# Optimization experiments

Measured on AMD Instinct MI355X. Metric: run time of the kernel, lower is better.

Reference implementation:

```python
import jax, jax.numpy as jnp
import numpy as np

HID, HEADS = 2048, 16
Q_LORA, KV_LORA = 1536, 512
NOPE, ROPE, VD = 128, 64, 128
N_EXP, TOPK, MOE_I, SH_I = 8, 2, 1408, 2816
EPS, RSF = 1e-6, 1.0
ROPE_BASE = 10000.0


def _rms(x, w):
    return x * jax.lax.rsqrt(jnp.mean(jnp.square(x), -1, keepdims=True) + EPS) * w


def _rope(x, pos):
    # neox-style rotary on last dim; x: [T, H, d], pos: [T]
    d = x.shape[-1]
    inv = 1.0 / (ROPE_BASE ** (jnp.arange(0, d, 2, dtype=jnp.float32) / d))
    ang = pos.astype(jnp.float32)[:, None] * inv  # [T, d/2]
    cos, sin = jnp.cos(ang)[:, None, :], jnp.sin(ang)[:, None, :]
    x1, x2 = x[..., : d // 2], x[..., d // 2:]
    return jnp.concatenate([x1 * cos - x2 * sin, x2 * cos + x1 * sin], -1)


def setup_inputs() -> dict:
    key = jax.random.key(0)
    ks = jax.random.split(key, 16)
    T, s, f = 1024, 0.02, jnp.float32
    return {
        'positions': jnp.arange(T, dtype=jnp.int32),
        'hidden_states': jax.random.normal(ks[0], (T, HID), f),
        'residual': jax.random.normal(ks[1], (T, HID), f),
        'w_in_ln': jnp.ones((HID,), f),
        'w_post_ln': jnp.ones((HID,), f),
        'w_q_ln': jnp.ones((Q_LORA,), f),
        'w_kv_ln': jnp.ones((KV_LORA,), f),
        'w_qkv_a': jax.random.normal(ks[2], (HID, Q_LORA + KV_LORA + ROPE), f) * s,
        'w_q_b': jax.random.normal(ks[3], (Q_LORA, HEADS * (NOPE + ROPE)), f) * s,
        'w_kv_b': jax.random.normal(ks[4], (KV_LORA, HEADS * (NOPE + VD)), f) * s,
        'w_o': jax.random.normal(ks[5], (HEADS * VD, HID), f) * s,
        'gate_w': jax.random.normal(ks[6], (HID, N_EXP), f) * s,
        'we_gate': jax.random.normal(ks[7], (N_EXP, HID, MOE_I), f) * s,
        'we_up': jax.random.normal(ks[8], (N_EXP, HID, MOE_I), f) * s,
        'we_down': jax.random.normal(ks[9], (N_EXP, MOE_I, HID), f) * s,
        'ws_gate': jax.random.normal(ks[10], (HID, SH_I), f) * s,
        'ws_up': jax.random.normal(ks[11], (HID, SH_I), f) * s,
        'ws_down': jax.random.normal(ks[12], (SH_I, HID), f) * s,
    }


def reference(positions, hidden_states, residual, w_in_ln, w_post_ln, w_q_ln, w_kv_ln,
              w_qkv_a, w_q_b, w_kv_b, w_o, gate_w, we_gate, we_up, we_down,
              ws_gate, ws_up, ws_down):
    T = hidden_states.shape[0]
    # fused_add_rms_norm: residual <- x + residual; x <- rmsnorm(residual)
    residual = hidden_states + residual
    h = _rms(residual, w_in_ln)
    # fused qkv_a projection and split
    qkv = h @ w_qkv_a  # [T, q_lora + kv_lora + rope]
    q_c = _rms(qkv[:, :Q_LORA], w_q_ln)
    kv_c = _rms(qkv[:, Q_LORA:Q_LORA + KV_LORA], w_kv_ln)
    k_pe = qkv[:, Q_LORA + KV_LORA:][:, None, :]  # [T, 1, rope]
    # MLA up-projections
    q = (q_c @ w_q_b).reshape(T, HEADS, NOPE + ROPE)
    q_nope, q_pe = q[..., :NOPE], q[..., NOPE:]
    kv = (kv_c @ w_kv_b).reshape(T, HEADS, NOPE + VD)
    k_nope, v = kv[..., :NOPE], kv[..., NOPE:]
    q_pe = _rope(q_pe, positions)
    k_pe = _rope(k_pe, positions)
    q = jnp.concatenate([q_nope, q_pe], -1)  # [T, H, nope+rope]
    k = jnp.concatenate([k_nope, jnp.broadcast_to(k_pe, (T, HEADS, ROPE))], -1)
    scores = jnp.einsum('qhd,khd->hqk', q, k) * (NOPE + ROPE) ** -0.5
    causal = jnp.tril(jnp.ones((T, T), bool))
    scores = jnp.where(causal, scores, jnp.finfo(scores.dtype).min)
    p = jax.nn.softmax(scores, -1)
    attn_out = jnp.einsum('hqk,khd->qhd', p, v).reshape(T, HEADS * VD) @ w_o
    # post-attention fused add + norm
    residual = residual + attn_out
    h = _rms(residual, w_post_ln)
    # MoE gate: softmax scores, top-k, renormalized combine weights
    probs = jax.nn.softmax(h @ gate_w, -1)
    tw, ti = jax.lax.top_k(probs, TOPK)
    tw = tw / jnp.sum(tw, -1, keepdims=True)
    comb = jnp.sum(jax.nn.one_hot(ti, N_EXP, dtype=h.dtype) * tw[..., None], 1)  # [T, E]
    # routed experts (dense grouped-GEMM reference, SwiGLU)
    g = jnp.einsum('th,ehi->eti', h, we_gate)
    u = jnp.einsum('th,ehi->eti', h, we_up)
    y = jnp.einsum('eti,eih->eth', jax.nn.silu(g) * u, we_down)
    routed = jnp.einsum('te,eth->th', comb, y) * RSF
    # shared experts
    shared = (jax.nn.silu(h @ ws_gate) * (h @ ws_up)) @ ws_down
    return routed + shared, residual
```

## Files before the change

kernel.cpp:

```cpp
#include <hip/hip_runtime.h>
#include <hip/hip_bf16.h>

typedef unsigned short u16;
typedef __attribute__((ext_vector_type(8))) short bf16x8;
typedef __attribute__((ext_vector_type(4))) float f32x4;
typedef __attribute__((ext_vector_type(8))) unsigned short u16x8;
typedef __attribute__((ext_vector_type(4))) unsigned short u16x4;

#define T_TOK 1024
#define HID 2048
#define HEADS 16
#define Q_LORA 1536
#define KV_LORA 512
#define NOPE 128
#define ROPED 64
#define VD 128
#define N_EXP 8
#define MOE_I 1408
#define SH_I 2816
#define QKV_N 2112
#define QKV_LD 2176
#define QD 192
#define KVD 256
#define EPSF 1e-6f
#define NEG_BIG (-3.4e38f)

__device__ __forceinline__ u16 f2bf(float f) {
  union { float f; unsigned u; } x; x.f = f;
  unsigned r = x.u + 0x7fffu + ((x.u >> 16) & 1u);
  return (u16)(r >> 16);
}
__device__ __forceinline__ float bf2f(u16 h) {
  union { unsigned u; float f; } x; x.u = ((unsigned)h) << 16; return x.f;
}
__device__ __forceinline__ void split2(float f, u16& hi, u16& lo) {
  hi = f2bf(f);
  lo = f2bf(f - bf2f(hi));
}

__device__ __forceinline__ void gload16(const u16* g, const u16* l) {
  __builtin_amdgcn_global_load_lds(
      (const __attribute__((address_space(1))) void*)g,
      (__attribute__((address_space(3))) void*)l, 16, 0, 0);
}

__device__ __forceinline__ float block_sum(float v, float* s) {
  #pragma unroll
  for (int o = 32; o > 0; o >>= 1) v += __shfl_down(v, o, 64);
  int w = threadIdx.x >> 6, lane = threadIdx.x & 63;
  __syncthreads();
  if (lane == 0) s[w] = v;
  __syncthreads();
  float r = s[0];
  for (int i = 1; i < 4; ++i) r += s[i];
  return r;
}
__device__ __forceinline__ float block_max(float v, float* s) {
  #pragma unroll
  for (int o = 32; o > 0; o >>= 1) v = fmaxf(v, __shfl_down(v, o, 64));
  int w = threadIdx.x >> 6, lane = threadIdx.x & 63;
  __syncthreads();
  if (lane == 0) s[w] = v;
  __syncthreads();
  float r = s[0];
  for (int i = 1; i < 4; ++i) r = fmaxf(r, s[i]);
  return r;
}

__global__ __launch_bounds__(256) void gemm_bf16(
    const u16* __restrict__ A, long asz, int lda,
    const u16* __restrict__ B, long bsz, int ldb,
    float* __restrict__ C, u16* __restrict__ Cb, long csz, int ldc,
    const float* __restrict__ Cadd, const u16* __restrict__ CaddB, int ldcadd,
    int K, float alpha, int causal, int mode,
    float* __restrict__ pbuf, int ksplit, int stot, int soff,
    const int* __restrict__ gidx, const int* __restrict__ gcnt) {
  const int bm = blockIdx.y << 7, bn = blockIdx.x << 7;
  const int zz = blockIdx.z;
  const int z = (ksplit > 1) ? (zz / ksplit) : zz;
  const int s = (ksplit > 1) ? (zz % ksplit) : 0;
  if (gcnt && bm >= gcnt[z]) return;
  A += (long)z * asz; B += (long)z * bsz;
  if (C) C += (long)z * csz;
  if (Cb) Cb += (long)z * csz;
  if (Cadd && !pbuf) Cadd += (long)z * csz;
  if (CaddB) CaddB += (long)z * csz;
  const int tid = threadIdx.x, lane = tid & 63, wid = tid >> 6;

  if (causal && bn >= bm + 128) return;

  __shared__ alignas(16) u16 As[2][128 * 32];
  __shared__ alignas(16) u16 Bs[2][128 * 32];

  const int wr = wid >> 1, wc = wid & 1;
  f32x4 acc[4][4];
  #pragma unroll
  for (int m = 0; m < 4; ++m)
    #pragma unroll
    for (int n = 0; n < 4; ++n) acc[m][n] = f32x4{0.f, 0.f, 0.f, 0.f};

  const int srow = (wid << 5) + (lane >> 2);
  const int scol = (lane & 3) << 3;
  const int arow = (wr << 6) + (lane & 15);
  const int brow = (wc << 6) + (lane & 15);
  const int koff = (lane >> 4) << 3;

  long ga0, ga1;
  {
    if (gidx) {
      const int* tk = gidx + (long)z * T_TOK;
      ga0 = (long)tk[bm + srow]; ga1 = (long)tk[bm + srow + 16];
    } else {
      ga0 = (long)(bm + srow); ga1 = (long)(bm + srow + 16);
    }
  }

  const int kseg = K / ksplit;
  const int kbeg = s * kseg;
  const int nIter = kseg >> 5;

  #define STAGE_TILE(BUF, KK)                                                 \
    {                                                                         \
      u16* asp = &As[(BUF)][(wid << 10)];                                     \
      u16* bsp = &Bs[(BUF)][(wid << 10)];                                     \
      gload16(A + ga0 * lda + (KK) + scol, asp);                              \
      gload16(A + ga1 * lda + (KK) + scol, asp + 512);                        \
      gload16(B + (long)(bn + srow) * ldb + (KK) + scol, bsp);                \
      gload16(B + (long)(bn + srow + 16) * ldb + (KK) + scol, bsp + 512);     \
    }

  STAGE_TILE(0, kbeg);
  __syncthreads();

  int cur = 0;
  for (int it = 0; it < nIter; ++it) {
    int k0 = kbeg + (it << 5);
    if (it + 1 < nIter) STAGE_TILE(cur ^ 1, k0 + 32);
    bf16x8 a[4], b[4];
    #pragma unroll
    for (int m = 0; m < 4; ++m) a[m] = *(const bf16x8*)&As[cur][((arow + (m << 4)) << 5) + koff];
    #pragma unroll
    for (int n = 0; n < 4; ++n) b[n] = *(const bf16x8*)&Bs[cur][((brow + (n << 4)) << 5) + koff];
    #pragma unroll
    for (int m = 0; m < 4; ++m)
      #pragma unroll
      for (int n = 0; n < 4; ++n)
        acc[m][n] = __builtin_amdgcn_mfma_f32_16x16x32_bf16(a[m], b[n], acc[m][n], 0, 0, 0);
    __syncthreads();
    cur ^= 1;
  }
  #undef STAGE_TILE

  const int rbase = bm + (wr << 6) + ((lane >> 4) << 2);
  const int cbase = bn + (wc << 6) + (lane & 15);

  if (pbuf) {
    long pstride = (long)(gridDim.y << 7) * ldc;
    float* pp = pbuf + ((long)z * stot + soff + s) * pstride;
    #pragma unroll
    for (int m = 0; m < 4; ++m)
      #pragma unroll
      for (int j = 0; j < 4; ++j) {
        int r = rbase + (m << 4) + j;
        #pragma unroll
        for (int n = 0; n < 4; ++n) {
          int cc = cbase + (n << 4);
          pp[(long)r * ldc + cc] = acc[m][n][j];
        }
      }
    return;
  }

  #pragma unroll
  for (int m = 0; m < 4; ++m) {
    #pragma unroll
    for (int j = 0; j < 4; ++j) {
      int r = rbase + (m << 4) + j;
      #pragma unroll
      for (int n = 0; n < 4; ++n) {
        int cc = cbase + (n << 4);
        float v = acc[m][n][j] * alpha;
        if (mode == 0) {
          if (Cadd) v += Cadd[(long)r * ldcadd + cc];
          if (causal && cc > r) v = NEG_BIG;
          C[(long)r * ldc + cc] = v;
        } else if (mode == 1) {
          float gg = Cadd[(long)r * ldcadd + cc];
          float sgv = gg / (1.f + expf(-gg));
          Cb[(long)r * ldc + cc] = f2bf(sgv * v);
        } else if (mode == 2) {
          Cb[(long)r * ldc + cc] = f2bf(v);
        } else {
          float gg = bf2f(CaddB[(long)r * ldcadd + cc]);
          float sgv = gg / (1.f + expf(-gg));
          Cb[(long)r * ldc + cc] = f2bf(sgv * v);
        }
      }
    }
  }
}

__global__ __launch_bounds__(256) void reduce_sk(
    const float* __restrict__ pbuf, long pstride, int S,
    float* __restrict__ C, u16* __restrict__ Cb, long csz, int ldc, int Nc,
    const float* __restrict__ Cadd, long caddsz, int ldcadd,
    float alpha, int mode) {
  const int z = blockIdx.y;
  const float* pz = pbuf + (long)z * S * pstride;
  long idx = ((long)blockIdx.x * 256 + threadIdx.x) * 8;
  long r = idx / Nc; int c = (int)(idx - r * Nc);
  float a[8] = {0.f, 0.f, 0.f, 0.f, 0.f, 0.f, 0.f, 0.f};
  for (int s = 0; s < S; ++s) {
    const float* pp = pz + (long)s * pstride + idx;
    float4 x = *(const float4*)pp;
    float4 y = *(const float4*)(pp + 4);
    a[0] += x.x; a[1] += x.y; a[2] += x.z; a[3] += x.w;
    a[4] += y.x; a[5] += y.y; a[6] += y.z; a[7] += y.w;
  }
  long ob = (long)z * csz + r * ldc + c;
  if (mode == 0) {
    #pragma unroll
    for (int k = 0; k < 8; ++k) {
      float v = a[k] * alpha;
      if (Cadd) v += Cadd[(long)z * caddsz + r * ldcadd + c + k];
      C[ob + k] = v;
    }
  } else {
    u16x8 o;
    #pragma unroll
    for (int k = 0; k < 8; ++k) {
      float gg = Cadd[(long)z * caddsz + r * ldcadd + c + k];
      float sgv = gg / (1.f + expf(-gg));
      o[k] = f2bf(sgv * a[k] * alpha);
    }
    *(u16x8*)&Cb[ob] = o;
  }
}

__global__ __launch_bounds__(256) void transpose_f32_bf16(
    const float* __restrict__ src, long sbs, int ld_src, int Cvalid,
    u16* __restrict__ dst, long dbs, int ld_dst) {
  __shared__ float tile[64][65];
  src += (long)blockIdx.z * sbs; dst += (long)blockIdx.z * dbs;
  const int c0 = blockIdx.x << 6, r0 = blockIdx.y << 6;
  const int tid = threadIdx.x;
  const int tc = (tid & 15) << 2, tr0 = tid >> 4;
  const bool valid = c0 < Cvalid;
  #pragma unroll
  for (int i = 0; i < 4; ++i) {
    int r = tr0 + (i << 4);
    float4 v;
    if (valid) v = *(const float4*)&src[(long)(r0 + r) * ld_src + c0 + tc];
    else { v.x = 0.f; v.y = 0.f; v.z = 0.f; v.w = 0.f; }
    tile[r][tc] = v.x; tile[r][tc + 1] = v.y; tile[r][tc + 2] = v.z; tile[r][tc + 3] = v.w;
  }
  __syncthreads();
  const int oc = tid >> 2, seg = tid & 3;
  u16x8 o0, o1;
  #pragma unroll
  for (int k = 0; k < 8; ++k) o0[k] = f2bf(tile[(seg << 4) + k][oc]);
  #pragma unroll
  for (int k = 0; k < 8; ++k) o1[k] = f2bf(tile[(seg << 4) + 8 + k][oc]);
  u16* dp = &dst[(long)(c0 + oc) * ld_dst + r0 + (seg << 4)];
  *(u16x8*)dp = o0;
  *(u16x8*)(dp + 8) = o1;
}

__global__ __launch_bounds__(256) void transpose_split3(
    const float* __restrict__ src, long sbs, int ld_src, int Cvalid,
    u16* __restrict__ dst, long dbs, int Kp) {
  __shared__ float tile[64][65];
  src += (long)blockIdx.z * sbs; dst += (long)blockIdx.z * dbs;
  const int c0 = blockIdx.x << 6, r0 = blockIdx.y << 6;
  const int tid = threadIdx.x;
  const int tc = (tid & 15) << 2, tr0 = tid >> 4;
  const bool valid = c0 < Cvalid;
  #pragma unroll
  for (int i = 0; i < 4; ++i) {
    int r = tr0 + (i << 4);
    float4 v;
    if (valid) v = *(const float4*)&src[(long)(r0 + r) * ld_src + c0 + tc];
    else { v.x = 0.f; v.y = 0.f; v.z = 0.f; v.w = 0.f; }
    tile[r][tc] = v.x; tile[r][tc + 1] = v.y; tile[r][tc + 2] = v.z; tile[r][tc + 3] = v.w;
  }
  __syncthreads();
  const int oc = tid >> 2, seg = tid & 3;
  u16x8 h0, h1, l0, l1;
  #pragma unroll
  for (int k = 0; k < 8; ++k) {
    u16 hi, lo; split2(tile[(seg << 4) + k][oc], hi, lo);
    h0[k] = hi; l0[k] = lo;
  }
  #pragma unroll
  for (int k = 0; k < 8; ++k) {
    u16 hi, lo; split2(tile[(seg << 4) + 8 + k][oc], hi, lo);
    h1[k] = hi; l1[k] = lo;
  }
  const int ldd = 3 * Kp;
  u16* dp = &dst[(long)(c0 + oc) * ldd + r0 + (seg << 4)];
  *(u16x8*)dp = h0;            *(u16x8*)(dp + 8) = h1;
  *(u16x8*)(dp + Kp) = h0;     *(u16x8*)(dp + Kp + 8) = h1;
  *(u16x8*)(dp + 2 * Kp) = l0; *(u16x8*)(dp + 2 * Kp + 8) = l1;
}

__global__ __launch_bounds__(256) void conv_split3_kernel(
    const float* __restrict__ src, u16* __restrict__ dst, int C, long n) {
  long stride = (long)gridDim.x * 2048;
  for (long i = ((long)blockIdx.x * 256 + threadIdx.x) * 8; i < n; i += stride) {
    long r = i / C; int c = (int)(i - r * C);
    float4 a = *(const float4*)&src[i];
    float4 b = *(const float4*)&src[i + 4];
    u16x8 hv, lv;
    u16 hi, lo;
    split2(a.x, hi, lo); hv[0] = hi; lv[0] = lo;
    split2(a.y, hi, lo); hv[1] = hi; lv[1] = lo;
    split2(a.z, hi, lo); hv[2] = hi; lv[2] = lo;
    split2(a.w, hi, lo); hv[3] = hi; lv[3] = lo;
    split2(b.x, hi, lo); hv[4] = hi; lv[4] = lo;
    split2(b.y, hi, lo); hv[5] = hi; lv[5] = lo;
    split2(b.z, hi, lo); hv[6] = hi; lv[6] = lo;
    split2(b.w, hi, lo); hv[7] = hi; lv[7] = lo;
    u16* base = dst + r * (long)(3 * C) + c;
    *(u16x8*)base = hv;
    *(u16x8*)(base + C) = lv;
    *(u16x8*)(base + 2 * C) = hv;
  }
}

__global__ __launch_bounds__(256) void add_rms_kernel(
    const float* __restrict__ hs, const float* __restrict__ res,
    const float* __restrict__ w, float* __restrict__ resid1, u16* __restrict__ h3) {
  __shared__ float sbuf[4];
  int t = blockIdx.x;
  float v[8]; float ss = 0.f;
  #pragma unroll
  for (int i = 0; i < 8; ++i) {
    int j = threadIdx.x + (i << 8);
    float x = hs[(long)t * HID + j] + res[(long)t * HID + j];
    v[i] = x; resid1[(long)t * HID + j] = x; ss += x * x;
  }
  ss = block_sum(ss, sbuf);
  float sc = rsqrtf(ss / (float)HID + EPSF);
  u16* base = h3 + (long)t * (3 * HID);
  #pragma unroll
  for (int i = 0; i < 8; ++i) {
    int j = threadIdx.x + (i << 8);
    u16 hi, lo; split2(v[i] * sc * w[j], hi, lo);
    base[j] = hi; base[HID + j] = lo; base[2 * HID + j] = hi;
  }
}

template <int NW, bool SPLIT, bool WF32>
__global__ __launch_bounds__(256) void rms_rows_kernel(
    const float* __restrict__ in, int ldin, const float* __restrict__ w,
    u16* __restrict__ outb, float* __restrict__ outf) {
  __shared__ float sbuf[4];
  int t = blockIdx.x;
  const int W = NW * 256;
  float v[NW]; float ss = 0.f;
  #pragma unroll
  for (int i = 0; i < NW; ++i) {
    int j = threadIdx.x + (i << 8);
    float x = in[(long)t * ldin + j];
    v[i] = x; ss += x * x;
  }
  ss = block_sum(ss, sbuf);
  float sc = rsqrtf(ss / (float)W + EPSF);
  #pragma unroll
  for (int i = 0; i < NW; ++i) {
    int j = threadIdx.x + (i << 8);
    float y = v[i] * sc * w[j];
    if (SPLIT) {
      u16 hi, lo; split2(y, hi, lo);
      u16* base = outb + (long)t * (3 * W);
      base[j] = hi; base[W + j] = lo; base[2 * W + j] = hi;
    } else {
      outb[(long)t * W + j] = f2bf(y);
    }
    if (WF32) outf[(long)t * W + j] = y;
  }
}

__global__ __launch_bounds__(256) void rope_kernel(
    const int* __restrict__ pos, float* __restrict__ q,
    const float* __restrict__ qkv, float* __restrict__ kpe) {
  int t = blockIdx.x;
  float fp = (float)pos[t];
  for (int item = threadIdx.x; item < 544; item += 256) {
    int i = item & 31;
    float inv = expf(-((float)i * (2.f / 64.f)) * 9.210340371976184f);
    float ang = fp * inv;
    float c = cosf(ang), s = sinf(ang);
    if (item < 512) {
      int hh = item >> 5;
      long base = (long)t * (HEADS * QD) + hh * QD + NOPE;
      float x1 = q[base + i], x2 = q[base + 32 + i];
      q[base + i] = x1 * c - x2 * s;
      q[base + 32 + i] = x2 * c + x1 * s;
    } else {
      long base = (long)t * QKV_LD + (Q_LORA + KV_LORA);
      float x1 = qkv[base + i], x2 = qkv[base + 32 + i];
      kpe[(long)t * 64 + i] = x1 * c - x2 * s;
      kpe[(long)t * 64 + 32 + i] = x2 * c + x1 * s;
    }
  }
}

__global__ __launch_bounds__(192) void build_q3_kernel(
    const float* __restrict__ qbuf, u16* __restrict__ q3) {
  int t = blockIdx.x, h = blockIdx.y, d = threadIdx.x;
  float x = qbuf[(long)t * (HEADS * QD) + h * QD + d];
  u16 hi, lo; split2(x, hi, lo);
  u16* base = q3 + ((long)h * T_TOK + t) * (3 * QD);
  base[d] = hi; base[QD + d] = lo; base[2 * QD + d] = hi;
}

__global__ __launch_bounds__(192) void build_kmat3_kernel(
    const float* __restrict__ kv, const float* __restrict__ kpe,
    u16* __restrict__ kmat3) {
  int t = blockIdx.x, h = blockIdx.y, d = threadIdx.x;
  float v = (d < NOPE) ? kv[(long)t * (HEADS * KVD) + h * KVD + d]
                       : kpe[(long)t * 64 + (d - NOPE)];
  u16 hi, lo; split2(v, hi, lo);
  u16* base = kmat3 + ((long)h * T_TOK + t) * (3 * QD);
  base[d] = hi; base[QD + d] = hi; base[2 * QD + d] = lo;
}

__global__ __launch_bounds__(256) void softmax_kernel(
    const float* __restrict__ S, u16* __restrict__ P2) {
  __shared__ float sbuf[4];
  long row = blockIdx.x;
  int r = (int)(row & (T_TOK - 1));
  const float* p = S + row * T_TOK;
  float4 v = ((const float4*)p)[threadIdx.x];
  int c0 = threadIdx.x << 2;
  if (c0 + 0 > r) v.x = NEG_BIG;
  if (c0 + 1 > r) v.y = NEG_BIG;
  if (c0 + 2 > r) v.z = NEG_BIG;
  if (c0 + 3 > r) v.w = NEG_BIG;
  float m = fmaxf(fmaxf(v.x, v.y), fmaxf(v.z, v.w));
  m = block_max(m, sbuf);
  v.x = expf(v.x - m); v.y = expf(v.y - m); v.z = expf(v.z - m); v.w = expf(v.w - m);
  float s = v.x + v.y + v.z + v.w;
  s = block_sum(s, sbuf);
  float inv = 1.f / s;
  u16x4 hv, lv;
  u16 hi, lo;
  split2(v.x * inv, hi, lo); hv[0] = hi; lv[0] = lo;
  split2(v.y * inv, hi, lo); hv[1] = hi; lv[1] = lo;
  split2(v.z * inv, hi, lo); hv[2] = hi; lv[2] = lo;
  split2(v.w * inv, hi, lo); hv[3] = hi; lv[3] = lo;
  u16* base = P2 + row * (2 * T_TOK) + (threadIdx.x << 2);
  *(u16x4*)base = hv;
  *(u16x4*)(base + T_TOK) = lv;
}

__global__ __launch_bounds__(256) void gate_topk_kernel(
    const float* __restrict__ h2, const float* __restrict__ gw,
    int* __restrict__ ti, float* __restrict__ tw) {
  __shared__ float sbuf[4];
  __shared__ float lg[N_EXP];
  int t = blockIdx.x;
  float p[N_EXP] = {0.f, 0.f, 0.f, 0.f, 0.f, 0.f, 0.f, 0.f};
  for (int j = threadIdx.x; j < HID; j += 256) {
    float x = h2[(long)t * HID + j];
    const float* gr = gw + (long)j * N_EXP;
    #pragma unroll
    for (int e = 0; e < N_EXP; ++e) p[e] += x * gr[e];
  }
  #pragma unroll
  for (int e = 0; e < N_EXP; ++e) {
    float s = block_sum(p[e], sbuf);
    if (threadIdx.x == 0) lg[e] = s;
  }
  __syncthreads();
  if (threadIdx.x == 0) {
    float m = lg[0];
    for (int e = 1; e < N_EXP; ++e) m = fmaxf(m, lg[e]);
    float pe[N_EXP]; float s = 0.f;
    for (int e = 0; e < N_EXP; ++e) { pe[e] = expf(lg[e] - m); s += pe[e]; }
    for (int e = 0; e < N_EXP; ++e) pe[e] /= s;
    int i0 = 0;
    for (int e = 1; e < N_EXP; ++e) if (pe[e] > pe[i0]) i0 = e;
    int i1 = -1;
    for (int e = 0; e < N_EXP; ++e) if (e != i0 && (i1 < 0 || pe[e] > pe[i1])) i1 = e;
    float ssum = pe[i0] + pe[i1];
    ti[2 * t] = i0; ti[2 * t + 1] = i1;
    tw[2 * t] = pe[i0] / ssum; tw[2 * t + 1] = pe[i1] / ssum;
  }
}

__global__ __launch_bounds__(64) void route_build_kernel(
    const int* __restrict__ ti, int* __restrict__ tokidx,
    int* __restrict__ pos, int* __restrict__ cnt) {
  int e = blockIdx.x;
  int le = (e < 10) ? e : e - 10;
  int lane = threadIdx.x;
  if (le >= N_EXP) {
    for (int p = lane; p < T_TOK; p += 64) tokidx[(long)e * T_TOK + p] = p;
    if (lane == 0) cnt[e] = T_TOK;
    return;
  }
  int c = 0;
  for (int base = 0; base < T_TOK; base += 64) {
    int t = base + lane;
    int e0 = ti[2 * t], e1 = ti[2 * t + 1];
    bool match = (e0 == le) || (e1 == le);
    unsigned long long mask = __ballot(match);
    int pref = __popcll(mask & ((1ull << lane) - 1ull));
    if (match) {
      int p = c + pref;
      tokidx[(long)e * T_TOK + p] = t;
      if (e < 10) pos[2 * t + ((e0 == le) ? 0 : 1)] = p;
    }
    c += __popcll(mask);
  }
  for (int p = c + lane; p < T_TOK; p += 64) tokidx[(long)e * T_TOK + p] = 0;
  if (lane == 0) cnt[e] = c;
}

__global__ __launch_bounds__(256) void silu_mul_moe_kernel(
    const u16* __restrict__ gug, const int* __restrict__ cnt,
    u16* __restrict__ gact) {
  int r = blockIdx.x, e = blockIdx.y;
  int padded = (cnt[e] + 127) & ~127;
  if (r >= padded) return;
  int j = threadIdx.x << 3;
  if (j >= MOE_I) return;
  u16x8 gv = *(const u16x8*)&gug[((long)e * T_TOK + r) * MOE_I + j];
  u16x8 uv = *(const u16x8*)&gug[(((long)e + 10) * T_TOK + r) * MOE_I + j];
  u16x8 o;
  #pragma unroll
  for (int k = 0; k < 8; ++k) {
    float g = bf2f(gv[k]);
    o[k] = f2bf(g / (1.f + expf(-g)) * bf2f(uv[k]));
  }
  *(u16x8*)&gact[((long)e * T_TOK + r) * MOE_I + j] = o;
}

__global__ __launch_bounds__(256) void combine_out_kernel(
    const u16* __restrict__ y, const int* __restrict__ ti,
    const float* __restrict__ tw, const int* __restrict__ pos,
    float* __restrict__ out0) {
  int t = blockIdx.x;
  int j = threadIdx.x << 3;
  int e0 = ti[2 * t], e1 = ti[2 * t + 1];
  int p0 = pos[2 * t], p1 = pos[2 * t + 1];
  float w0 = tw[2 * t], w1 = tw[2 * t + 1];
  u16x8 a = *(const u16x8*)&y[((long)e0 * T_TOK + p0) * HID + j];
  u16x8 b = *(const u16x8*)&y[((long)e1 * T_TOK + p1) * HID + j];
  u16x8 c = *(const u16x8*)&y[((long)8 * T_TOK + t) * HID + j];
  u16x8 d = *(const u16x8*)&y[((long)9 * T_TOK + t) * HID + j];
  float* rp = out0 + (long)t * HID + j;
  #pragma unroll
  for (int k = 0; k < 8; ++k)
    rp[k] = w0 * bf2f(a[k]) + w1 * bf2f(b[k]) + bf2f(c[k]) + bf2f(d[k]);
}

extern "C" void kernel_launch(void* const* d_in, const int* in_sizes, int n_in,
                              void* d_out, int out_size, void* d_ws, size_t ws_size,
                              hipStream_t stream) {
  (void)in_sizes; (void)n_in; (void)out_size; (void)ws_size;
  const int*   positions = (const int*)d_in[0];
  const float* hs        = (const float*)d_in[1];
  const float* res       = (const float*)d_in[2];
  const float* w_in_ln   = (const float*)d_in[3];
  const float* w_post_ln = (const float*)d_in[4];
  const float* w_q_ln    = (const float*)d_in[5];
  const float* w_kv_ln   = (const float*)d_in[6];
  const float* w_qkv_a   = (const float*)d_in[7];
  const float* w_q_b     = (const float*)d_in[8];
  const float* w_kv_b    = (const float*)d_in[9];
  const float* w_o       = (const float*)d_in[10];
  const float* gate_w    = (const float*)d_in[11];
  const float* we_gate   = (const float*)d_in[12];
  const float* we_up     = (const float*)d_in[13];
  const float* we_down   = (const float*)d_in[14];
  const float* ws_gate   = (const float*)d_in[15];
  const float* ws_up     = (const float*)d_in[16];
  const float* ws_dn     = (const float*)d_in[17];

  float* out0   = (float*)d_out;
  float* resid2 = out0 + (long)T_TOK * HID;

  char* Wb = (char*)d_ws;
  size_t off = 0;
  #define CARVE(name, type, bytes) type* name = (type*)(Wb + off); off += (((size_t)(bytes) + 255) & ~(size_t)255)

  CARVE(wqkvaT3, u16, (size_t)QKV_LD * 3 * HID * 2);
  CARVE(wqbT3,   u16, (size_t)(HEADS * QD) * 3 * Q_LORA * 2);
  CARVE(wkvbT3,  u16, (size_t)(HEADS * KVD) * 3 * KV_LORA * 2);
  CARVE(woT3,    u16, (size_t)HID * 3 * HID * 2);

  size_t pool = off;
  CARVE(resid1, float, (size_t)T_TOK * HID * 4);
  CARVE(h3,     u16,   (size_t)T_TOK * 3 * HID * 2);
  CARVE(qkv,    float, (size_t)T_TOK * QKV_LD * 4);
  CARVE(qc3,    u16,   (size_t)T_TOK * 3 * Q_LORA * 2);
  CARVE(kvc3,   u16,   (size_t)T_TOK * 3 * KV_LORA * 2);
  CARVE(qbuf,   float, (size_t)T_TOK * HEADS * QD * 4);
  CARVE(q3,     u16,   (size_t)HEADS * T_TOK * 3 * QD * 2);
  CARVE(kvbuf,  float, (size_t)T_TOK * HEADS * KVD * 4);
  CARVE(kpe,    float, (size_t)T_TOK * 64 * 4);
  CARVE(kmat3,  u16,   (size_t)HEADS * T_TOK * 3 * QD * 2);
  CARVE(vt3,    u16,   (size_t)HEADS * VD * 3 * T_TOK * 2);
  CARVE(scores, float, (size_t)HEADS * T_TOK * T_TOK * 4);
  CARVE(P2,     u16,   (size_t)HEADS * T_TOK * 2 * T_TOK * 2);
  CARVE(attn,   float, (size_t)T_TOK * HID * 4);
  CARVE(attn3,  u16,   (size_t)T_TOK * 3 * HID * 2);
  size_t endA = off;
  float* pbufA = scores;

  off = pool;
  CARVE(wegu20, u16, (size_t)20 * MOE_I * HID * 2);
  CARVE(wedT10, u16, (size_t)10 * HID * MOE_I * 2);
  CARVE(h2,     float, (size_t)T_TOK * HID * 4);
  CARVE(h2_b,   u16,   (size_t)T_TOK * HID * 2);
  CARVE(ti,     int,   (size_t)T_TOK * 2 * 4);
  CARVE(tw,     float, (size_t)T_TOK * 2 * 4);
  CARVE(pos,    int,   (size_t)T_TOK * 2 * 4);
  CARVE(tokidx20, int, (size_t)20 * T_TOK * 4);
  CARVE(cnt20,  int,   128);
  CARVE(gug20,  u16,   (size_t)20 * T_TOK * MOE_I * 2);
  CARVE(gact,   u16,   (size_t)10 * T_TOK * MOE_I * 2);
  CARVE(ycomp,  u16,   (size_t)10 * T_TOK * HID * 2);
  if (off < endA) off = endA;
  #undef CARVE

  u16* wegT10 = wegu20;
  u16* weuT10 = wegu20 + (size_t)10 * MOE_I * HID;

  const float* nullf = nullptr;
  float* nullC = nullptr;
  u16* nullB = nullptr;
  const u16* nullBB = nullptr;
  const int* nullI = nullptr;

  hipLaunchKernelGGL(transpose_split3, dim3(QKV_LD / 64, HID / 64, 1), dim3(256), 0, stream,
                     w_qkv_a, 0L, QKV_N, QKV_N, wqkvaT3, 0L, HID);
  hipLaunchKernelGGL(transpose_split3, dim3(HEADS * QD / 64, Q_LORA / 64, 1), dim3(256), 0, stream,
                     w_q_b, 0L, HEADS * QD, HEADS * QD, wqbT3, 0L, Q_LORA);
  hipLaunchKernelGGL(transpose_split3, dim3(HEADS * KVD / 64, KV_LORA / 64, 1), dim3(256), 0, stream,
                     w_kv_b, 0L, HEADS * KVD, HEADS * KVD, wkvbT3, 0L, KV_LORA);
  hipLaunchKernelGGL(transpose_split3, dim3(HID / 64, HID / 64, 1), dim3(256), 0, stream,
                     w_o, 0L, HID, HID, woT3, 0L, HID);

  hipLaunchKernelGGL(add_rms_kernel, dim3(T_TOK), dim3(256), 0, stream,
                     hs, res, w_in_ln, resid1, h3);
  hipLaunchKernelGGL(gemm_bf16, dim3(QKV_LD / 128, T_TOK / 128, 4), dim3(256), 0, stream,
                     h3, 0L, 3 * HID, wqkvaT3, 0L, 3 * HID,
                     nullC, nullB, 0L, QKV_LD, nullf, nullBB, 0, 3 * HID, 1.f, 0, 0,
                     pbufA, 4, 4, 0, nullI, nullI);
  hipLaunchKernelGGL(reduce_sk, dim3(T_TOK * QKV_LD / 2048, 1), dim3(256), 0, stream,
                     pbufA, (long)T_TOK * QKV_LD, 4,
                     qkv, nullB, 0L, QKV_LD, QKV_LD, nullf, 0L, 0, 1.f, 0);
  hipLaunchKernelGGL((rms_rows_kernel<6, true, false>), dim3(T_TOK), dim3(256), 0, stream,
                     qkv, QKV_LD, w_q_ln, qc3, (float*)nullptr);
  hipLaunchKernelGGL((rms_rows_kernel<2, true, false>), dim3(T_TOK), dim3(256), 0, stream,
                     qkv + Q_LORA, QKV_LD, w_kv_ln, kvc3, (float*)nullptr);
  hipLaunchKernelGGL(gemm_bf16, dim3(HEADS * QD / 128, T_TOK / 128, 4), dim3(256), 0, stream,
                     qc3, 0L, 3 * Q_LORA, wqbT3, 0L, 3 * Q_LORA,
                     nullC, nullB, 0L, HEADS * QD, nullf, nullBB, 0, 3 * Q_LORA, 1.f, 0, 0,
                     pbufA, 4, 4, 0, nullI, nullI);
  hipLaunchKernelGGL(reduce_sk, dim3(T_TOK * HEADS * QD / 2048, 1), dim3(256), 0, stream,
                     pbufA, (long)T_TOK * HEADS * QD, 4,
                     qbuf, nullB, 0L, HEADS * QD, HEADS * QD, nullf, 0L, 0, 1.f, 0);
  hipLaunchKernelGGL(gemm_bf16, dim3(HEADS * KVD / 128, T_TOK / 128, 4), dim3(256), 0, stream,
                     kvc3, 0L, 3 * KV_LORA, wkvbT3, 0L, 3 * KV_LORA,
                     nullC, nullB, 0L, HEADS * KVD, nullf, nullBB, 0, 3 * KV_LORA, 1.f, 0, 0,
                     pbufA, 4, 4, 0, nullI, nullI);
  hipLaunchKernelGGL(reduce_sk, dim3(T_TOK * HEADS * KVD / 2048, 1), dim3(256), 0, stream,
                     pbufA, (long)T_TOK * HEADS * KVD, 4,
                     kvbuf, nullB, 0L, HEADS * KVD, HEADS * KVD, nullf, 0L, 0, 1.f, 0);
  hipLaunchKernelGGL(rope_kernel, dim3(T_TOK), dim3(256), 0, stream,
                     positions, qbuf, qkv, kpe);
  hipLaunchKernelGGL(build_q3_kernel, dim3(T_TOK, HEADS), dim3(192), 0, stream, qbuf, q3);
  hipLaunchKernelGGL(build_kmat3_kernel, dim3(T_TOK, HEADS), dim3(192), 0, stream,
                     kvbuf, kpe, kmat3);
  hipLaunchKernelGGL(transpose_split3, dim3(VD / 64, T_TOK / 64, HEADS), dim3(256), 0, stream,
                     kvbuf + NOPE, 256L, HEADS * KVD, VD, vt3, (long)VD * 3 * T_TOK, T_TOK);
  hipLaunchKernelGGL(gemm_bf16, dim3(T_TOK / 128, T_TOK / 128, HEADS), dim3(256), 0, stream,
                     q3, (long)T_TOK * 3 * QD, 3 * QD,
                     kmat3, (long)T_TOK * 3 * QD, 3 * QD,
                     scores, nullB, (long)T_TOK * T_TOK, T_TOK,
                     nullf, nullBB, 0, 576, 0.07216878364870322f, 1, 0,
                     nullC, 1, 1, 0, nullI, nullI);
  hipLaunchKernelGGL(softmax_kernel, dim3(HEADS * T_TOK), dim3(256), 0, stream, scores, P2);
  hipLaunchKernelGGL(gemm_bf16, dim3(VD / 128, T_TOK / 128, HEADS * 4), dim3(256), 0, stream,
                     P2, (long)T_TOK * 2 * T_TOK, 2 * T_TOK,
                     vt3, (long)VD * 3 * T_TOK, 3 * T_TOK,
                     nullC, nullB, 0L, VD, nullf, nullBB, 0, 2 * T_TOK, 1.f, 0, 0,
                     pbufA, 4, 6, 0, nullI, nullI);
  hipLaunchKernelGGL(gemm_bf16, dim3(VD / 128, T_TOK / 128, HEADS * 2), dim3(256), 0, stream,
                     P2, (long)T_TOK * 2 * T_TOK, 2 * T_TOK,
                     vt3 + 2 * T_TOK, (long)VD * 3 * T_TOK, 3 * T_TOK,
                     nullC, nullB, 0L, VD, nullf, nullBB, 0, T_TOK, 1.f, 0, 0,
                     pbufA, 2, 6, 4, nullI, nullI);
  hipLaunchKernelGGL(reduce_sk, dim3(T_TOK * VD / 2048, HEADS), dim3(256), 0, stream,
                     pbufA, (long)T_TOK * VD, 6,
                     attn, nullB, (long)VD, HID, VD, nullf, 0L, 0, 1.f, 0);
  hipLaunchKernelGGL(conv_split3_kernel, dim3(1024), dim3(256), 0, stream,
                     attn, attn3, HID, (long)T_TOK * HID);
  hipLaunchKernelGGL(gemm_bf16, dim3(HID / 128, T_TOK / 128, 4), dim3(256), 0, stream,
                     attn3, 0L, 3 * HID, woT3, 0L, 3 * HID,
                     nullC, nullB, 0L, HID, nullf, nullBB, 0, 3 * HID, 1.f, 0, 0,
                     pbufA, 4, 4, 0, nullI, nullI);
  hipLaunchKernelGGL(reduce_sk, dim3(T_TOK * HID / 2048, 1), dim3(256), 0, stream,
                     pbufA, (long)T_TOK * HID, 4,
                     resid2, nullB, 0L, HID, HID, resid1, 0L, HID, 1.f, 0);

  hipLaunchKernelGGL(transpose_f32_bf16, dim3(MOE_I / 64, HID / 64, N_EXP), dim3(256), 0, stream,
                     we_gate, (long)HID * MOE_I, MOE_I, MOE_I, wegT10, (long)MOE_I * HID, HID);
  hipLaunchKernelGGL(transpose_f32_bf16, dim3(MOE_I / 64, HID / 64, 2), dim3(256), 0, stream,
                     ws_gate, (long)MOE_I, SH_I, MOE_I,
                     wegT10 + (size_t)8 * MOE_I * HID, (long)MOE_I * HID, HID);
  hipLaunchKernelGGL(transpose_f32_bf16, dim3(MOE_I / 64, HID / 64, N_EXP), dim3(256), 0, stream,
                     we_up, (long)HID * MOE_I, MOE_I, MOE_I, weuT10, (long)MOE_I * HID, HID);
  hipLaunchKernelGGL(transpose_f32_bf16, dim3(MOE_I / 64, HID / 64, 2), dim3(256), 0, stream,
                     ws_up, (long)MOE_I, SH_I, MOE_I,
                     weuT10 + (size_t)8 * MOE_I * HID, (long)MOE_I * HID, HID);
  hipLaunchKernelGGL(transpose_f32_bf16, dim3(HID / 64, MOE_I / 64, N_EXP), dim3(256), 0, stream,
                     we_down, (long)MOE_I * HID, HID, HID, wedT10, (long)HID * MOE_I, MOE_I);
  hipLaunchKernelGGL(transpose_f32_bf16, dim3(HID / 64, MOE_I / 64, 2), dim3(256), 0, stream,
                     ws_dn, (long)MOE_I * HID, HID, HID,
                     wedT10 + (size_t)8 * HID * MOE_I, (long)HID * MOE_I, MOE_I);

  hipLaunchKernelGGL((rms_rows_kernel<8, false, true>), dim3(T_TOK), dim3(256), 0, stream,
                     resid2, HID, w_post_ln, h2_b, h2);
  hipLaunchKernelGGL(gate_topk_kernel, dim3(T_TOK), dim3(256), 0, stream,
                     h2, gate_w, ti, tw);
  hipLaunchKernelGGL(route_build_kernel, dim3(20), dim3(64), 0, stream,
                     ti, tokidx20, pos, cnt20);
  hipLaunchKernelGGL(gemm_bf16, dim3(MOE_I / 128, T_TOK / 128, 20), dim3(256), 0, stream,
                     h2_b, 0L, HID, wegu20, (long)MOE_I * HID, HID,
                     nullC, gug20, (long)T_TOK * MOE_I, MOE_I,
                     nullf, nullBB, 0, HID, 1.f, 0, 2, nullC, 1, 1, 0, tokidx20, cnt20);
  hipLaunchKernelGGL(silu_mul_moe_kernel, dim3(T_TOK, 10), dim3(256), 0, stream,
                     gug20, cnt20, gact);
  hipLaunchKernelGGL(gemm_bf16, dim3(HID / 128, T_TOK / 128, 10), dim3(256), 0, stream,
                     gact, (long)T_TOK * MOE_I, MOE_I,
                     wedT10, (long)HID * MOE_I, MOE_I,
                     nullC, ycomp, (long)T_TOK * HID, HID,
                     nullf, nullBB, 0, MOE_I, 1.f, 0, 2, nullC, 1, 1, 0, nullI, cnt20);
  hipLaunchKernelGGL(combine_out_kernel, dim3(T_TOK), dim3(256), 0, stream,
                     ycomp, ti, tw, pos, out0);
}
```

Measured before the change: 827.5 us.

## Skip masked causal K-blocks in PV GEMM and fuse split conversion into reduce

Adds a kcap parameter to the GEMM so the P·V products stop their K loop at the causal diagonal, skipping tiles of probabilities that are zero. The attention split-K reduce now writes the hi/lo/hi bf16 split layout directly, removing the fp32 attn buffer and the separate conversion kernel. Softmax also skips loading score values that are fully masked. The risk is that the segment base arithmetic for the 2x-wide P2 layout must line up with T_TOK boundaries, and any mismatch would drop needed terms.

```diff
diff --git a/kernel.cpp b/kernel.cpp
--- a/kernel.cpp
+++ b/kernel.cpp
@@ -74,7 +74,7 @@
     const float* __restrict__ Cadd, const u16* __restrict__ CaddB, int ldcadd,
     int K, float alpha, int causal, int mode,
     float* __restrict__ pbuf, int ksplit, int stot, int soff,
-    const int* __restrict__ gidx, const int* __restrict__ gcnt) {
+    const int* __restrict__ gidx, const int* __restrict__ gcnt, int kcap) {
   const int bm = blockIdx.y << 7, bn = blockIdx.x << 7;
   const int zz = blockIdx.z;
   const int z = (ksplit > 1) ? (zz / ksplit) : zz;
@@ -117,7 +117,14 @@
 
   const int kseg = K / ksplit;
   const int kbeg = s * kseg;
-  const int nIter = kseg >> 5;
+  int kend = kbeg + kseg;
+  if (kcap) {
+    int segbase = (kbeg / T_TOK) * T_TOK;
+    int cap = segbase + bm + 128;
+    if (kend > cap) kend = cap;
+  }
+  int nIter = (kend - kbeg) >> 5;
+  if (nIter < 0) nIter = 0;
 
   #define STAGE_TILE(BUF, KK)                                                 \
     {                                                                         \
@@ -129,25 +136,27 @@
       gload16(B + (long)(bn + srow + 16) * ldb + (KK) + scol, bsp + 512);     \
     }
 
-  STAGE_TILE(0, kbeg);
-  __syncthreads();
-
-  int cur = 0;
-  for (int it = 0; it < nIter; ++it) {
-    int k0 = kbeg + (it << 5);
-    if (it + 1 < nIter) STAGE_TILE(cur ^ 1, k0 + 32);
-    bf16x8 a[4], b[4];
-    #pragma unroll
-    for (int m = 0; m < 4; ++m) a[m] = *(const bf16x8*)&As[cur][((arow + (m << 4)) << 5) + koff];
-    #pragma unroll
-    for (int n = 0; n < 4; ++n) b[n] = *(const bf16x8*)&Bs[cur][((brow + (n << 4)) << 5) + koff];
-    #pragma unroll
-    for (int m = 0; m < 4; ++m)
+  if (nIter > 0) {
+    STAGE_TILE(0, kbeg);
+    __syncthreads();
+
+    int cur = 0;
+    for (int it = 0; it < nIter; ++it) {
+      int k0 = kbeg + (it << 5);
+      if (it + 1 < nIter) STAGE_TILE(cur ^ 1, k0 + 32);
+      bf16x8 a[4], b[4];
       #pragma unroll
-      for (int n = 0; n < 4; ++n)
-        acc[m][n] = __builtin_amdgcn_mfma_f32_16x16x32_bf16(a[m], b[n], acc[m][n], 0, 0, 0);
-    __syncthreads();
-    cur ^= 1;
+      for (int m = 0; m < 4; ++m) a[m] = *(const bf16x8*)&As[cur][((arow + (m << 4)) << 5) + koff];
+      #pragma unroll
+      for (int n = 0; n < 4; ++n) b[n] = *(const bf16x8*)&Bs[cur][((brow + (n << 4)) << 5) + koff];
+      #pragma unroll
+      for (int m = 0; m < 4; ++m)
+        #pragma unroll
+        for (int n = 0; n < 4; ++n)
+          acc[m][n] = __builtin_amdgcn_mfma_f32_16x16x32_bf16(a[m], b[n], acc[m][n], 0, 0, 0);
+      __syncthreads();
+      cur ^= 1;
+    }
   }
   #undef STAGE_TILE
 
@@ -217,15 +226,16 @@
     a[0] += x.x; a[1] += x.y; a[2] += x.z; a[3] += x.w;
     a[4] += y.x; a[5] += y.y; a[6] += y.z; a[7] += y.w;
   }
-  long ob = (long)z * csz + r * ldc + c;
   if (mode == 0) {
+    long ob = (long)z * csz + r * ldc + c;
     #pragma unroll
     for (int k = 0; k < 8; ++k) {
       float v = a[k] * alpha;
       if (Cadd) v += Cadd[(long)z * caddsz + r * ldcadd + c + k];
       C[ob + k] = v;
     }
-  } else {
+  } else if (mode == 1) {
+    long ob = (long)z * csz + r * ldc + c;
     u16x8 o;
     #pragma unroll
     for (int k = 0; k < 8; ++k) {
@@ -234,6 +244,17 @@
       o[k] = f2bf(sgv * a[k] * alpha);
     }
     *(u16x8*)&Cb[ob] = o;
+  } else {
+    long base = r * (3L * ldc) + (long)z * csz + c;
+    u16x8 hv, lv;
+    #pragma unroll
+    for (int k = 0; k < 8; ++k) {
+      u16 hi, lo; split2(a[k] * alpha, hi, lo);
+      hv[k] = hi; lv[k] = lo;
+    }
+    *(u16x8*)&Cb[base] = hv;
+    *(u16x8*)&Cb[base + ldc] = lv;
+    *(u16x8*)&Cb[base + 2 * ldc] = hv;
   }
 }
 
@@ -301,30 +322,6 @@
   *(u16x8*)dp = h0;            *(u16x8*)(dp + 8) = h1;
   *(u16x8*)(dp + Kp) = h0;     *(u16x8*)(dp + Kp + 8) = h1;
   *(u16x8*)(dp + 2 * Kp) = l0; *(u16x8*)(dp + 2 * Kp + 8) = l1;
-}
-
-__global__ __launch_bounds__(256) void conv_split3_kernel(
-    const float* __restrict__ src, u16* __restrict__ dst, int C, long n) {
-  long stride = (long)gridDim.x * 2048;
-  for (long i = ((long)blockIdx.x * 256 + threadIdx.x) * 8; i < n; i += stride) {
-    long r = i / C; int c = (int)(i - r * C);
-    float4 a = *(const float4*)&src[i];
-    float4 b = *(const float4*)&src[i + 4];
-    u16x8 hv, lv;
-    u16 hi, lo;
-    split2(a.x, hi, lo); hv[0] = hi; lv[0] = lo;
-    split2(a.y, hi, lo); hv[1] = hi; lv[1] = lo;
-    split2(a.z, hi, lo); hv[2] = hi; lv[2] = lo;
-    split2(a.w, hi, lo); hv[3] = hi; lv[3] = lo;
-    split2(b.x, hi, lo); hv[4] = hi; lv[4] = lo;
-    split2(b.y, hi, lo); hv[5] = hi; lv[5] = lo;
-    split2(b.z, hi, lo); hv[6] = hi; lv[6] = lo;
-    split2(b.w, hi, lo); hv[7] = hi; lv[7] = lo;
-    u16* base = dst + r * (long)(3 * C) + c;
-    *(u16x8*)base = hv;
-    *(u16x8*)(base + C) = lv;
-    *(u16x8*)(base + 2 * C) = hv;
-  }
 }
 
 __global__ __launch_bounds__(256) void add_rms_kernel(
@@ -432,12 +429,16 @@
   long row = blockIdx.x;
   int r = (int)(row & (T_TOK - 1));
   const float* p = S + row * T_TOK;
-  float4 v = ((const float4*)p)[threadIdx.x];
   int c0 = threadIdx.x << 2;
-  if (c0 + 0 > r) v.x = NEG_BIG;
-  if (c0 + 1 > r) v.y = NEG_BIG;
-  if (c0 + 2 > r) v.z = NEG_BIG;
-  if (c0 + 3 > r) v.w = NEG_BIG;
+  float4 v;
+  if (c0 <= r) {
+    v = ((const float4*)p)[threadIdx.x];
+    if (c0 + 1 > r) v.y = NEG_BIG;
+    if (c0 + 2 > r) v.z = NEG_BIG;
+    if (c0 + 3 > r) v.w = NEG_BIG;
+  } else {
+    v.x = NEG_BIG; v.y = NEG_BIG; v.z = NEG_BIG; v.w = NEG_BIG;
+  }
   float m = fmaxf(fmaxf(v.x, v.y), fmaxf(v.z, v.w));
   m = block_max(m, sbuf);
   v.x = expf(v.x - m); v.y = expf(v.y - m); v.z = expf(v.z - m); v.w = expf(v.w - m);
@@ -606,7 +607,6 @@
   CARVE(vt3,    u16,   (size_t)HEADS * VD * 3 * T_TOK * 2);
   CARVE(scores, float, (size_t)HEADS * T_TOK * T_TOK * 4);
   CARVE(P2,     u16,   (size_t)HEADS * T_TOK * 2 * T_TOK * 2);
-  CARVE(attn,   float, (size_t)T_TOK * HID * 4);
   CARVE(attn3,  u16,   (size_t)T_TOK * 3 * HID * 2);
   size_t endA = off;
   float* pbufA = scores;
@@ -650,7 +650,7 @@
   hipLaunchKernelGGL(gemm_bf16, dim3(QKV_LD / 128, T_TOK / 128, 4), dim3(256), 0, stream,
                      h3, 0L, 3 * HID, wqkvaT3, 0L, 3 * HID,
                      nullC, nullB, 0L, QKV_LD, nullf, nullBB, 0, 3 * HID, 1.f, 0, 0,
-                     pbufA, 4, 4, 0, nullI, nullI);
+                     pbufA, 4, 4, 0, nullI, nullI, 0);
   hipLaunchKernelGGL(reduce_sk, dim3(T_TOK * QKV_LD / 2048, 1), dim3(256), 0, stream,
                      pbufA, (long)T_TOK * QKV_LD, 4,
                      qkv, nullB, 0L, QKV_LD, QKV_LD, nullf, 0L, 0, 1.f, 0);
@@ -661,14 +661,14 @@
   hipLaunchKernelGGL(gemm_bf16, dim3(HEADS * QD / 128, T_TOK / 128, 4), dim3(256), 0, stream,
                      qc3, 0L, 3 * Q_LORA, wqbT3, 0L, 3 * Q_LORA,
                      nullC, nullB, 0L, HEADS * QD, nullf, nullBB, 0, 3 * Q_LORA, 1.f, 0, 0,
-                     pbufA, 4, 4, 0, nullI, nullI);
+                     pbufA, 4, 4, 0, nullI, nullI, 0);
   hipLaunchKernelGGL(reduce_sk, dim3(T_TOK * HEADS * QD / 2048, 1), dim3(256), 0, stream,
                      pbufA, (long)T_TOK * HEADS * QD, 4,
                      qbuf, nullB, 0L, HEADS * QD, HEADS * QD, nullf, 0L, 0, 1.f, 0);
   hipLaunchKernelGGL(gemm_bf16, dim3(HEADS * KVD / 128, T_TOK / 128, 4), dim3(256), 0, stream,
                      kvc3, 0L, 3 * KV_LORA, wkvbT3, 0L, 3 * KV_LORA,
                      nullC, nullB, 0L, HEADS * KVD, nullf, nullBB, 0, 3 * KV_LORA, 1.f, 0, 0,
-                     pbufA, 4, 4, 0, nullI, nullI);
+                     pbufA, 4, 4, 0, nullI, nullI, 0);
   hipLaunchKernelGGL(reduce_sk, dim3(T_TOK * HEADS * KVD / 2048, 1), dim3(256), 0, stream,
                      pbufA, (long)T_TOK * HEADS * KVD, 4,
                      kvbuf, nullB, 0L, HEADS * KVD, HEADS * KVD, nullf, 0L, 0, 1.f, 0);
@@ -684,27 +684,25 @@
                      kmat3, (long)T_TOK * 3 * QD, 3 * QD,
                      scores, nullB, (long)T_TOK * T_TOK, T_TOK,
                      nullf, nullBB, 0, 576, 0.07216878364870322f, 1, 0,
-                     nullC, 1, 1, 0, nullI, nullI);
+                     nullC, 1, 1, 0, nullI, nullI, 0);
   hipLaunchKernelGGL(softmax_kernel, dim3(HEADS * T_TOK), dim3(256), 0, stream, scores, P2);
   hipLaunchKernelGGL(gemm_bf16, dim3(VD / 128, T_TOK / 128, HEADS * 4), dim3(256), 0, stream,
                      P2, (long)T_TOK * 2 * T_TOK, 2 * T_TOK,
                      vt3, (long)VD * 3 * T_TOK, 3 * T_TOK,
                      nullC, nullB, 0L, VD, nullf, nullBB, 0, 2 * T_TOK, 1.f, 0, 0,
-                     pbufA, 4, 6, 0, nullI, nullI);
+                     pbufA, 4, 6, 0, nullI, nullI, 1);
   hipLaunchKernelGGL(gemm_bf16, dim3(VD / 128, T_TOK / 128, HEADS * 2), dim3(256), 0, stream,
                      P2, (long)T_TOK * 2 * T_TOK, 2 * T_TOK,
                      vt3 + 2 * T_TOK, (long)VD * 3 * T_TOK, 3 * T_TOK,
                      nullC, nullB, 0L, VD, nullf, nullBB, 0, T_TOK, 1.f, 0, 0,
-                     pbufA, 2, 6, 4, nullI, nullI);
+                     pbufA, 2, 6, 4, nullI, nullI, 1);
   hipLaunchKernelGGL(reduce_sk, dim3(T_TOK * VD / 2048, HEADS), dim3(256), 0, stream,
                      pbufA, (long)T_TOK * VD, 6,
-                     attn, nullB, (long)VD, HID, VD, nullf, 0L, 0, 1.f, 0);
-  hipLaunchKernelGGL(conv_split3_kernel, dim3(1024), dim3(256), 0, stream,
-                     attn, attn3, HID, (long)T_TOK * HID);
+                     nullC, attn3, (long)VD, HID, VD, nullf, 0L, 0, 1.f, 2);
   hipLaunchKernelGGL(gemm_bf16, dim3(HID / 128, T_TOK / 128, 4), dim3(256), 0, stream,
                      attn3, 0L, 3 * HID, woT3, 0L, 3 * HID,
                      nullC, nullB, 0L, HID, nullf, nullBB, 0, 3 * HID, 1.f, 0, 0,
-                     pbufA, 4, 4, 0, nullI, nullI);
+                     pbufA, 4, 4, 0, nullI, nullI, 0);
   hipLaunchKernelGGL(reduce_sk, dim3(T_TOK * HID / 2048, 1), dim3(256), 0, stream,
                      pbufA, (long)T_TOK * HID, 4,
                      resid2, nullB, 0L, HID, HID, resid1, 0L, HID, 1.f, 0);
@@ -734,14 +732,14 @@
   hipLaunchKernelGGL(gemm_bf16, dim3(MOE_I / 128, T_TOK / 128, 20), dim3(256), 0, stream,
                      h2_b, 0L, HID, wegu20, (long)MOE_I * HID, HID,
                      nullC, gug20, (long)T_TOK * MOE_I, MOE_I,
-                     nullf, nullBB, 0, HID, 1.f, 0, 2, nullC, 1, 1, 0, tokidx20, cnt20);
+                     nullf, nullBB, 0, HID, 1.f, 0, 2, nullC, 1, 1, 0, tokidx20, cnt20, 0);
   hipLaunchKernelGGL(silu_mul_moe_kernel, dim3(T_TOK, 10), dim3(256), 0, stream,
                      gug20, cnt20, gact);
   hipLaunchKernelGGL(gemm_bf16, dim3(HID / 128, T_TOK / 128, 10), dim3(256), 0, stream,
                      gact, (long)T_TOK * MOE_I, MOE_I,
                      wedT10, (long)HID * MOE_I, MOE_I,
                      nullC, ycomp, (long)T_TOK * HID, HID,
-                     nullf, nullBB, 0, MOE_I, 1.f, 0, 2, nullC, 1, 1, 0, nullI, cnt20);
+                     nullf, nullBB, 0, MOE_I, 1.f, 0, 2, nullC, 1, 1, 0, nullI, cnt20, 0);
   hipLaunchKernelGGL(combine_out_kernel, dim3(T_TOK), dim3(256), 0, stream,
                      ycomp, ti, tw, pos, out0);
 }
```

Measured after the change: 812.6 us (median of 2 runs). Within noise of the previous version (-1.8%).
